# Kernel optimization log

Hardware: AMD Instinct MI355X
Metric: run time of the kernel (lower is better)

Reference implementation:

```python
import jax, jax.numpy as jnp
import numpy as np

ALPHA = 0.95
GAMMA = 8.0
REFRACTORY_STEPS = 2.0
THETA_INC = 0.35
THETA_DECAY = 0.995

B, N, T = 16, 2048, 1000


def setup_inputs() -> dict:
    key = jax.random.key(0)
    u = jax.random.normal(key, (B, N, T), dtype=jnp.float32)
    theta_base = jnp.ones((1, N, 1), dtype=jnp.float32)
    return {"u": u, "theta_base": theta_base}


def surrogate_spike(x):
    # forward: Heaviside (x >= 0); surrogate grad handled in fwdbwd module
    return (x >= 0).astype(x.dtype)


def reference(u, theta_base):
    # u: [B, N, T]; theta_base: [1, N, 1]
    b, n, t = u.shape
    tb = theta_base[0, :, 0]  # [N], broadcasts over batch
    v0 = jnp.zeros((b, n), dtype=u.dtype)
    theta0 = jnp.broadcast_to(tb, (b, n)).astype(u.dtype)
    ref0 = jnp.zeros((b, n), dtype=u.dtype)

    def step(carry, u_t):
        v, theta_dyn, ref = carry
        ref_active = (ref > 0).astype(u_t.dtype)
        u_eff = u_t * (1.0 - ref_active)
        v = ALPHA * v + u_eff
        theta = theta_dyn  # adaptive_theta=True
        s = surrogate_spike(v - theta)
        v = v - s * theta  # soft reset (hard_reset=False)
        ref = jnp.maximum(ref - 1.0, 0.0)
        ref = jnp.where(s > 0, jnp.full_like(ref, REFRACTORY_STEPS), ref)
        theta_dyn = theta_dyn * THETA_DECAY + tb * (1.0 - THETA_DECAY) + THETA_INC * s
        return (v, theta_dyn, ref), (s, v)

    u_t_first = jnp.transpose(u, (2, 0, 1))  # [T, B, N]
    _, (spikes, v_hist) = jax.lax.scan(step, (v0, theta0, ref0), u_t_first)
    spikes = jnp.transpose(spikes, (1, 2, 0))  # [B, N, T]
    v_hist = jnp.transpose(v_hist, (1, 2, 0))
    return spikes, v_hist
```

## Files before the change

kernel.cpp:

```cpp
#include <hip/hip_runtime.h>


constexpr int B_ = 16;
constexpr int N_ = 2048;
constexpr int T_ = 1000;
constexpr int CHUNK = 64;
constexpr int NF4 = CHUNK / 4;
constexpr int NFULL = 15;
constexpr int NPAIR = 7;
constexpr int TAIL_T0 = NFULL * CHUNK;
constexpr int TAIL_F4 = (T_ - TAIL_T0) / 4;

#define LDS_BARRIER()                                          \
    do {                                                       \
        asm volatile("s_waitcnt lgkmcnt(0)" ::: "memory");     \
        __builtin_amdgcn_s_barrier();                          \
    } while (0)

__global__ __launch_bounds__(192) void lif_kernel(
    const float* __restrict__ u,
    const float* __restrict__ theta_base,
    float* __restrict__ spikes,
    float* __restrict__ vhist)
{
    __shared__ float4 s_lds[2][64][NF4];
    __shared__ float4 v_lds[2][64][NF4];

    const int lane = threadIdx.x & 63;
    const int wid = threadIdx.x >> 6;
    const int blk0 = blockIdx.x * 64;
    const size_t row = (size_t)(blk0 + lane) * T_;

    if (wid == 0) {
        const float tb = theta_base[(blk0 + lane) & (N_ - 1)];
        const float c5 = __fmul_rn(tb, 0.005f);
        float v = 0.0f, theta = tb, ref = 0.0f;
        const float* up = u + row;

        float4 bufA[NF4], bufB[NF4];

        auto load_full = [&](float4 (&buf)[NF4], int t0) {
#pragma unroll
            for (int i = 0; i < NF4; ++i)
                buf[i] = *reinterpret_cast<const float4*>(up + t0 + 4 * i);
        };
        auto load_tail = [&](float4 (&buf)[NF4]) {
#pragma unroll
            for (int i = 0; i < TAIL_F4; ++i)
                buf[i] = *reinterpret_cast<const float4*>(up + TAIL_T0 + 4 * i);
        };

        auto step4 = [&](const float4 u4, int par, int tf) {
            const float uin[4] = {u4.x, u4.y, u4.z, u4.w};
            float so[4], vo[4];
#pragma unroll
            for (int k = 0; k < 4; ++k) {
                const float ueff = (ref > 0.0f) ? 0.0f : uin[k];
                v = __fadd_rn(__fmul_rn(0.95f, v), ueff);
                const float d = __fsub_rn(v, theta);
                const bool s = (d >= 0.0f);
                v = s ? __fsub_rn(v, theta) : v;
                ref = fmaxf(__fsub_rn(ref, 1.0f), 0.0f);
                ref = s ? 2.0f : ref;
                theta = __fadd_rn(__fmul_rn(theta, 0.995f), c5);
                theta = s ? __fadd_rn(theta, 0.35f) : theta;

                so[k] = s ? 1.0f : 0.0f;
                vo[k] = v;
            }
            const int ptf = tf ^ (lane & 15);
            s_lds[par][lane][ptf] = make_float4(so[0], so[1], so[2], so[3]);
            v_lds[par][lane][ptf] = make_float4(vo[0], vo[1], vo[2], vo[3]);
        };

        auto process_full = [&](const float4 (&buf)[NF4], int par) {
#pragma unroll
            for (int tf = 0; tf < NF4; ++tf) step4(buf[tf], par, tf);
        };
        auto process_tail = [&](const float4 (&buf)[NF4], int par) {
#pragma unroll
            for (int tf = 0; tf < TAIL_F4; ++tf) step4(buf[tf], par, tf);
        };

        load_full(bufA, 0);
        int t = 0;
#pragma unroll 1
        for (int p = 0; p < NPAIR; ++p) {
            load_full(bufB, t + CHUNK);
            process_full(bufA, 0);
            LDS_BARRIER();
            t += CHUNK;
            load_full(bufA, t + CHUNK);
            process_full(bufB, 1);
            LDS_BARRIER();
            t += CHUNK;
        }
        load_tail(bufB);
        process_full(bufA, 0);
        LDS_BARRIER();
        process_tail(bufB, 1);
        LDS_BARRIER();
    } else {
        float* gout = (wid == 1) ? spikes : vhist;
        const float4 (*src)[64][NF4] = (wid == 1) ? s_lds : v_lds;
        float* gp = gout + (size_t)blk0 * T_;

        const int tf = lane & 15;
        const int rsub = lane >> 4;

#pragma unroll 1
        for (int c = 0; c < NFULL + 1; ++c) {
            if (c > 0) {
                const int par = (c - 1) & 1;
                const int t0 = (c - 1) * CHUNK;
#pragma unroll
                for (int k = 0; k < 16; ++k) {
                    const int r = 4 * k + rsub;
                    const float4 w = src[par][r][tf ^ (r & 15)];
                    *reinterpret_cast<float4*>(gp + (size_t)r * T_ + t0 + 4 * tf) = w;
                }
            }
            LDS_BARRIER();
        }
        {
#pragma unroll
            for (int j = 0; j < TAIL_F4; ++j) {
                const float4 w = src[1][lane][j ^ (lane & 15)];
                *reinterpret_cast<float4*>(gp + (size_t)lane * T_ + TAIL_T0 + 4 * j) = w;
            }
        }
    }
}

extern "C" void kernel_launch(void* const* d_in, const int* in_sizes, int n_in,
                              void* d_out, int out_size, void* d_ws, size_t ws_size,
                              hipStream_t stream) {
    const float* u = (const float*)d_in[0];
    const float* theta_base = (const float*)d_in[1];
    float* out = (float*)d_out;
    float* spikes = out;
    float* vhist = out + (size_t)B_ * N_ * T_;

    const int grid = (B_ * N_) / 64;
    lif_kernel<<<grid, 192, 0, stream>>>(u, theta_base, spikes, vhist);
}
```

Before: 109.8 us.

## Move input loads to a dedicated wave using async global-to-LDS triple buffering

Wave 1 now issues direct global-to-LDS loads of u for a three-deep ring of 32-step chunks, with coalesced row-group access and XOR swizzling. Wave 0 only reads from LDS and runs the recurrence, and wave 2 writes both spikes and v_hist. The aim is to keep the serial compute wave from stalling on strided per-row global loads and to free its registers. In exchange the chunks are half the size, so there are twice as many block barriers, and one writer wave now handles both outputs.

```diff
diff --git a/kernel.cpp b/kernel.cpp
--- a/kernel.cpp
+++ b/kernel.cpp
@@ -4,10 +4,9 @@
 constexpr int B_ = 16;
 constexpr int N_ = 2048;
 constexpr int T_ = 1000;
-constexpr int CHUNK = 64;
+constexpr int CHUNK = 32;
 constexpr int NF4 = CHUNK / 4;
-constexpr int NFULL = 15;
-constexpr int NPAIR = 7;
+constexpr int NFULL = 31;
 constexpr int TAIL_T0 = NFULL * CHUNK;
 constexpr int TAIL_F4 = (T_ - TAIL_T0) / 4;
 
@@ -15,7 +14,14 @@
     do {                                                       \
         asm volatile("s_waitcnt lgkmcnt(0)" ::: "memory");     \
         __builtin_amdgcn_s_barrier();                          \
+        __builtin_amdgcn_sched_barrier(0);                     \
     } while (0)
+
+__device__ __forceinline__ void gload_lds16(const float* g, void* lds) {
+    __builtin_amdgcn_global_load_lds(
+        (const __attribute__((address_space(1))) void*)g,
+        (__attribute__((address_space(3))) void*)lds, 16, 0, 0);
+}
 
 __global__ __launch_bounds__(192) void lif_kernel(
     const float* __restrict__ u,
@@ -23,34 +29,21 @@
     float* __restrict__ spikes,
     float* __restrict__ vhist)
 {
-    __shared__ float4 s_lds[2][64][NF4];
-    __shared__ float4 v_lds[2][64][NF4];
+    __shared__ float4 u_lds[3][64][NF4];
+    __shared__ float4 s_lds[3][64][NF4];
+    __shared__ float4 v_lds[3][64][NF4];
 
     const int lane = threadIdx.x & 63;
     const int wid = threadIdx.x >> 6;
     const int blk0 = blockIdx.x * 64;
-    const size_t row = (size_t)(blk0 + lane) * T_;
 
     if (wid == 0) {
         const float tb = theta_base[(blk0 + lane) & (N_ - 1)];
         const float c5 = __fmul_rn(tb, 0.005f);
         float v = 0.0f, theta = tb, ref = 0.0f;
-        const float* up = u + row;
+        const int sw = lane & 7;
 
-        float4 bufA[NF4], bufB[NF4];
-
-        auto load_full = [&](float4 (&buf)[NF4], int t0) {
-#pragma unroll
-            for (int i = 0; i < NF4; ++i)
-                buf[i] = *reinterpret_cast<const float4*>(up + t0 + 4 * i);
-        };
-        auto load_tail = [&](float4 (&buf)[NF4]) {
-#pragma unroll
-            for (int i = 0; i < TAIL_F4; ++i)
-                buf[i] = *reinterpret_cast<const float4*>(up + TAIL_T0 + 4 * i);
-        };
-
-        auto step4 = [&](const float4 u4, int par, int tf) {
+        auto step4 = [&](const float4 u4, float4& s4, float4& v4) {
             const float uin[4] = {u4.x, u4.y, u4.z, u4.w};
             float so[4], vo[4];
 #pragma unroll
@@ -68,65 +61,123 @@
                 so[k] = s ? 1.0f : 0.0f;
                 vo[k] = v;
             }
-            const int ptf = tf ^ (lane & 15);
-            s_lds[par][lane][ptf] = make_float4(so[0], so[1], so[2], so[3]);
-            v_lds[par][lane][ptf] = make_float4(vo[0], vo[1], vo[2], vo[3]);
+            s4 = make_float4(so[0], so[1], so[2], so[3]);
+            v4 = make_float4(vo[0], vo[1], vo[2], vo[3]);
         };
 
-        auto process_full = [&](const float4 (&buf)[NF4], int par) {
+        __builtin_amdgcn_s_barrier();
+        int bu = 0;
+#pragma unroll 1
+        for (int c = 0; c < NFULL; ++c) {
+            const float4* urow = &u_lds[bu][lane][0];
+            float4* srow = &s_lds[bu][lane][0];
+            float4* vrow = &v_lds[bu][lane][0];
 #pragma unroll
-            for (int tf = 0; tf < NF4; ++tf) step4(buf[tf], par, tf);
+            for (int tf = 0; tf < NF4; ++tf) {
+                float4 s4, v4;
+                step4(urow[tf ^ sw], s4, v4);
+                srow[tf ^ sw] = s4;
+                vrow[tf ^ sw] = v4;
+            }
+            LDS_BARRIER();
+            bu = (bu == 2) ? 0 : bu + 1;
+        }
+        {
+            const float4* ut = &u_lds[bu][0][0];
+            float4* st = &s_lds[bu][0][0];
+            float4* vt = &v_lds[bu][0][0];
+#pragma unroll
+            for (int tf = 0; tf < TAIL_F4; ++tf) {
+                float4 s4, v4;
+                step4(ut[TAIL_F4 * lane + tf], s4, v4);
+                st[TAIL_F4 * lane + tf] = s4;
+                vt[TAIL_F4 * lane + tf] = v4;
+            }
+            LDS_BARRIER();
+        }
+    } else if (wid == 1) {
+        const float* ub = u + (size_t)blk0 * T_;
+        const int r0 = lane >> 3;
+        const int sl = lane & 7;
+
+        auto issue_full = [&](int cc, int buf) {
+#pragma unroll
+            for (int k = 0; k < 8; ++k) {
+                const int r = 8 * k + r0;
+                const float* g =
+                    ub + (size_t)r * T_ + CHUNK * cc + 4 * (sl ^ (r & 7));
+                gload_lds16(g, &u_lds[buf][8 * k][0]);
+            }
         };
-        auto process_tail = [&](const float4 (&buf)[NF4], int par) {
+        auto issue_tail = [&]() {
 #pragma unroll
-            for (int tf = 0; tf < TAIL_F4; ++tf) step4(buf[tf], par, tf);
+            for (int j = 0; j < 2; ++j) {
+                const int r = 32 * j + (lane >> 1);
+                const int tf = lane & 1;
+                const float* g = ub + (size_t)r * T_ + TAIL_T0 + 4 * tf;
+                gload_lds16(g, ((float4*)&u_lds[1][0][0]) + 64 * j);
+            }
         };
 
-        load_full(bufA, 0);
-        int t = 0;
-#pragma unroll 1
-        for (int p = 0; p < NPAIR; ++p) {
-            load_full(bufB, t + CHUNK);
-            process_full(bufA, 0);
-            LDS_BARRIER();
-            t += CHUNK;
-            load_full(bufA, t + CHUNK);
-            process_full(bufB, 1);
-            LDS_BARRIER();
-            t += CHUNK;
-        }
-        load_tail(bufB);
-        process_full(bufA, 0);
-        LDS_BARRIER();
-        process_tail(bufB, 1);
-        LDS_BARRIER();
-    } else {
-        float* gout = (wid == 1) ? spikes : vhist;
-        const float4 (*src)[64][NF4] = (wid == 1) ? s_lds : v_lds;
-        float* gp = gout + (size_t)blk0 * T_;
-
-        const int tf = lane & 15;
-        const int rsub = lane >> 4;
-
+        issue_full(0, 0);
+        issue_full(1, 1);
+        asm volatile("s_waitcnt vmcnt(8)" ::: "memory");
+        __builtin_amdgcn_sched_barrier(0);
+        __builtin_amdgcn_s_barrier();
 #pragma unroll 1
         for (int c = 0; c < NFULL + 1; ++c) {
-            if (c > 0) {
-                const int par = (c - 1) & 1;
-                const int t0 = (c - 1) * CHUNK;
+            if (c <= 28) {
+                issue_full(c + 2, (c + 2) % 3);
+                asm volatile("s_waitcnt vmcnt(8)" ::: "memory");
+            } else if (c == 29) {
+                issue_tail();
+                asm volatile("s_waitcnt vmcnt(2)" ::: "memory");
+            } else if (c == 30) {
+                asm volatile("s_waitcnt vmcnt(0)" ::: "memory");
+            }
+            __builtin_amdgcn_sched_barrier(0);
+            __builtin_amdgcn_s_barrier();
+            __builtin_amdgcn_sched_barrier(0);
+        }
+    } else {
+        float* gs = spikes + (size_t)blk0 * T_;
+        float* gv = vhist + (size_t)blk0 * T_;
+        const int r0 = lane >> 3;
+        const int tfp = lane & 7;
+
+        __builtin_amdgcn_s_barrier();
+#pragma unroll 1
+        for (int c = 0; c < NFULL + 1; ++c) {
+            if (c >= 1) {
+                const int cc = c - 1;
+                const int buf = cc % 3;
+                const int t0 = CHUNK * cc;
 #pragma unroll
-                for (int k = 0; k < 16; ++k) {
-                    const int r = 4 * k + rsub;
-                    const float4 w = src[par][r][tf ^ (r & 15)];
-                    *reinterpret_cast<float4*>(gp + (size_t)r * T_ + t0 + 4 * tf) = w;
+                for (int k = 0; k < 8; ++k) {
+                    const int r = 8 * k + r0;
+                    const float4 w = s_lds[buf][r][tfp ^ (r & 7)];
+                    *(float4*)(gs + (size_t)r * T_ + t0 + 4 * tfp) = w;
+                }
+#pragma unroll
+                for (int k = 0; k < 8; ++k) {
+                    const int r = 8 * k + r0;
+                    const float4 w = v_lds[buf][r][tfp ^ (r & 7)];
+                    *(float4*)(gv + (size_t)r * T_ + t0 + 4 * tfp) = w;
                 }
             }
             LDS_BARRIER();
         }
         {
+            const float4* st = &s_lds[1][0][0];
+            const float4* vt = &v_lds[1][0][0];
 #pragma unroll
-            for (int j = 0; j < TAIL_F4; ++j) {
-                const float4 w = src[1][lane][j ^ (lane & 15)];
-                *reinterpret_cast<float4*>(gp + (size_t)lane * T_ + TAIL_T0 + 4 * j) = w;
+            for (int j = 0; j < 2; ++j) {
+                const int r = 32 * j + (lane >> 1);
+                const int tf = lane & 1;
+                *(float4*)(gs + (size_t)r * T_ + TAIL_T0 + 4 * tf) =
+                    st[64 * j + lane];
+                *(float4*)(gv + (size_t)r * T_ + TAIL_T0 + 4 * tf) =
+                    vt[64 * j + lane];
             }
         }
     }
```

Result: slower. 126.8 us (+15.4%).

## Pack spikes as bitmasks in LDS and drain 128-step chunks from 4-slot ring

Applied to the files above, without the earlier changes.

The compute wave now writes spikes as 64-bit bitmasks per row per 64-step chunk instead of float4s, which cuts LDS traffic for spikes. Voltage goes into a 4-slot LDS ring buffer. The two writer waves now drain two chunks (128 time steps) every other phase, so each row's store segment is 512 bytes rather than 256. This aims to give better global write coalescing and fewer writer iterations, at the cost of more LDS and of expanding the bits back to floats in the spike writer.

```diff
diff --git a/kernel.cpp b/kernel.cpp
--- a/kernel.cpp
+++ b/kernel.cpp
@@ -4,17 +4,16 @@
 constexpr int B_ = 16;
 constexpr int N_ = 2048;
 constexpr int T_ = 1000;
-constexpr int CHUNK = 64;
-constexpr int NF4 = CHUNK / 4;
-constexpr int NFULL = 15;
-constexpr int NPAIR = 7;
-constexpr int TAIL_T0 = NFULL * CHUNK;
-constexpr int TAIL_F4 = (T_ - TAIL_T0) / 4;
+constexpr int Q = 64;
+constexpr int QF4 = Q / 4;
+constexpr int NPH = 16;
+constexpr int TAIL_F4 = 10;
 
 #define LDS_BARRIER()                                          \
     do {                                                       \
         asm volatile("s_waitcnt lgkmcnt(0)" ::: "memory");     \
         __builtin_amdgcn_s_barrier();                          \
+        __builtin_amdgcn_sched_barrier(0);                     \
     } while (0)
 
 __global__ __launch_bounds__(192) void lif_kernel(
@@ -23,36 +22,36 @@
     float* __restrict__ spikes,
     float* __restrict__ vhist)
 {
-    __shared__ float4 s_lds[2][64][NF4];
-    __shared__ float4 v_lds[2][64][NF4];
+    __shared__ float4 v_ring[4][64][QF4];
+    __shared__ uint2  s_bits[4][64];
 
     const int lane = threadIdx.x & 63;
     const int wid = threadIdx.x >> 6;
     const int blk0 = blockIdx.x * 64;
-    const size_t row = (size_t)(blk0 + lane) * T_;
 
     if (wid == 0) {
         const float tb = theta_base[(blk0 + lane) & (N_ - 1)];
         const float c5 = __fmul_rn(tb, 0.005f);
         float v = 0.0f, theta = tb, ref = 0.0f;
-        const float* up = u + row;
-
-        float4 bufA[NF4], bufB[NF4];
-
-        auto load_full = [&](float4 (&buf)[NF4], int t0) {
-#pragma unroll
-            for (int i = 0; i < NF4; ++i)
-                buf[i] = *reinterpret_cast<const float4*>(up + t0 + 4 * i);
-        };
-        auto load_tail = [&](float4 (&buf)[NF4]) {
+        const float* up = u + (size_t)(blk0 + lane) * T_;
+        const int swz = lane & 15;
+
+        float4 bufA[QF4], bufB[QF4];
+
+        auto load_q = [&](float4 (&b)[QF4], int t0) {
+#pragma unroll
+            for (int i = 0; i < QF4; ++i)
+                b[i] = *reinterpret_cast<const float4*>(up + t0 + 4 * i);
+        };
+        auto load_tail = [&](float4 (&b)[QF4]) {
 #pragma unroll
             for (int i = 0; i < TAIL_F4; ++i)
-                buf[i] = *reinterpret_cast<const float4*>(up + TAIL_T0 + 4 * i);
-        };
-
-        auto step4 = [&](const float4 u4, int par, int tf) {
+                b[i] = *reinterpret_cast<const float4*>(up + 15 * Q + 4 * i);
+        };
+
+        auto stepf4 = [&](const float4 u4, unsigned& bw, int sh) -> float4 {
             const float uin[4] = {u4.x, u4.y, u4.z, u4.w};
-            float so[4], vo[4];
+            float vo[4];
 #pragma unroll
             for (int k = 0; k < 4; ++k) {
                 const float ueff = (ref > 0.0f) ? 0.0f : uin[k];
@@ -65,68 +64,140 @@
                 theta = __fadd_rn(__fmul_rn(theta, 0.995f), c5);
                 theta = s ? __fadd_rn(theta, 0.35f) : theta;
 
-                so[k] = s ? 1.0f : 0.0f;
+                bw |= (s ? 1u : 0u) << (sh + k);
                 vo[k] = v;
             }
-            const int ptf = tf ^ (lane & 15);
-            s_lds[par][lane][ptf] = make_float4(so[0], so[1], so[2], so[3]);
-            v_lds[par][lane][ptf] = make_float4(vo[0], vo[1], vo[2], vo[3]);
-        };
-
-        auto process_full = [&](const float4 (&buf)[NF4], int par) {
-#pragma unroll
-            for (int tf = 0; tf < NF4; ++tf) step4(buf[tf], par, tf);
-        };
-        auto process_tail = [&](const float4 (&buf)[NF4], int par) {
-#pragma unroll
-            for (int tf = 0; tf < TAIL_F4; ++tf) step4(buf[tf], par, tf);
-        };
-
-        load_full(bufA, 0);
-        int t = 0;
+            return make_float4(vo[0], vo[1], vo[2], vo[3]);
+        };
+
+        auto process_q = [&](const float4 (&b)[QF4], int bq) {
+            unsigned blo = 0, bhi = 0;
+#pragma unroll
+            for (int tf = 0; tf < QF4; ++tf) {
+                float4 v4 = (tf < 8) ? stepf4(b[tf], blo, 4 * tf)
+                                     : stepf4(b[tf], bhi, 4 * (tf - 8));
+                v_ring[bq][lane][tf ^ swz] = v4;
+            }
+            s_bits[bq][lane] = make_uint2(blo, bhi);
+        };
+        auto process_tail = [&](const float4 (&b)[QF4], int bq) {
+            unsigned blo = 0, bhi = 0;
+#pragma unroll
+            for (int tf = 0; tf < TAIL_F4; ++tf) {
+                float4 v4 = (tf < 8) ? stepf4(b[tf], blo, 4 * tf)
+                                     : stepf4(b[tf], bhi, 4 * (tf - 8));
+                v_ring[bq][lane][tf ^ swz] = v4;
+            }
+            s_bits[bq][lane] = make_uint2(blo, bhi);
+        };
+
+        load_q(bufA, 0);
 #pragma unroll 1
-        for (int p = 0; p < NPAIR; ++p) {
-            load_full(bufB, t + CHUNK);
-            process_full(bufA, 0);
+        for (int p = 0; p < NPH; ++p) {
+            if (!(p & 1)) {
+                if (p < 14) load_q(bufB, (p + 1) * Q);
+                else if (p == 14) load_tail(bufB);
+                process_q(bufA, p & 3);
+            } else {
+                if (p < 15) {
+                    load_q(bufA, (p + 1) * Q);
+                    process_q(bufB, p & 3);
+                } else {
+                    process_tail(bufB, 3);
+                }
+            }
             LDS_BARRIER();
-            t += CHUNK;
-            load_full(bufA, t + CHUNK);
-            process_full(bufB, 1);
+        }
+    } else if (wid == 1) {
+        float* gv = vhist + (size_t)blk0 * T_;
+        const int jj = lane & 31;
+        const int half = lane >> 5;
+
+#pragma unroll 1
+        for (int p = 0; p < NPH; ++p) {
+            if (p >= 2 && !(p & 1)) {
+                const int t0 = (p - 2) * Q;
+                const int b0 = (p - 2) & 3;
+                const int bq = (b0 + (jj >> 4)) & 3;
+                const int slb = jj & 15;
+#pragma unroll
+                for (int k = 0; k < 32; ++k) {
+                    const int R = 2 * k + half;
+                    const float4 w = v_ring[bq][R][slb ^ (R & 15)];
+                    *(float4*)(gv + (size_t)R * T_ + t0 + 4 * jj) = w;
+                }
+            }
             LDS_BARRIER();
-            t += CHUNK;
-        }
-        load_tail(bufB);
-        process_full(bufA, 0);
-        LDS_BARRIER();
-        process_tail(bufB, 1);
-        LDS_BARRIER();
+        }
+        {
+            const int r0 = lane >> 4, tf = lane & 15;
+#pragma unroll
+            for (int k = 0; k < 16; ++k) {
+                const int R = 4 * k + r0;
+                const float4 w = v_ring[2][R][tf ^ (R & 15)];
+                *(float4*)(gv + (size_t)R * T_ + 14 * Q + 4 * tf) = w;
+            }
+        }
+        {
+#pragma unroll
+            for (int tf = 0; tf < TAIL_F4; ++tf) {
+                const float4 w = v_ring[3][lane][tf ^ (lane & 15)];
+                *(float4*)(gv + (size_t)lane * T_ + 15 * Q + 4 * tf) = w;
+            }
+        }
     } else {
-        float* gout = (wid == 1) ? spikes : vhist;
-        const float4 (*src)[64][NF4] = (wid == 1) ? s_lds : v_lds;
-        float* gp = gout + (size_t)blk0 * T_;
-
-        const int tf = lane & 15;
-        const int rsub = lane >> 4;
+        float* gs = spikes + (size_t)blk0 * T_;
+        const int jj = lane & 31;
+        const int half = lane >> 5;
+
+        auto expand = [](unsigned w, int ob) -> float4 {
+            float4 f;
+            f.x = ((w >> (ob + 0)) & 1u) ? 1.0f : 0.0f;
+            f.y = ((w >> (ob + 1)) & 1u) ? 1.0f : 0.0f;
+            f.z = ((w >> (ob + 2)) & 1u) ? 1.0f : 0.0f;
+            f.w = ((w >> (ob + 3)) & 1u) ? 1.0f : 0.0f;
+            return f;
+        };
 
 #pragma unroll 1
-        for (int c = 0; c < NFULL + 1; ++c) {
-            if (c > 0) {
-                const int par = (c - 1) & 1;
-                const int t0 = (c - 1) * CHUNK;
-#pragma unroll
-                for (int k = 0; k < 16; ++k) {
-                    const int r = 4 * k + rsub;
-                    const float4 w = src[par][r][tf ^ (r & 15)];
-                    *reinterpret_cast<float4*>(gp + (size_t)r * T_ + t0 + 4 * tf) = w;
+        for (int p = 0; p < NPH; ++p) {
+            if (p >= 2 && !(p & 1)) {
+                const int t0 = (p - 2) * Q;
+                const int b0 = (p - 2) & 3;
+                const int bq = (b0 + (jj >> 4)) & 3;
+                const int wq = (jj & 15) >> 3;
+                const int ob = 4 * (jj & 7);
+#pragma unroll
+                for (int k = 0; k < 32; ++k) {
+                    const int R = 2 * k + half;
+                    const uint2 bw = s_bits[bq][R];
+                    const unsigned w = wq ? bw.y : bw.x;
+                    *(float4*)(gs + (size_t)R * T_ + t0 + 4 * jj) =
+                        expand(w, ob);
                 }
             }
             LDS_BARRIER();
         }
         {
-#pragma unroll
-            for (int j = 0; j < TAIL_F4; ++j) {
-                const float4 w = src[1][lane][j ^ (lane & 15)];
-                *reinterpret_cast<float4*>(gp + (size_t)lane * T_ + TAIL_T0 + 4 * j) = w;
+            const int r0 = lane >> 4, tf = lane & 15;
+            const int wq = tf >> 3;
+            const int ob = 4 * (tf & 7);
+#pragma unroll
+            for (int k = 0; k < 16; ++k) {
+                const int R = 4 * k + r0;
+                const uint2 bw = s_bits[2][R];
+                const unsigned w = wq ? bw.y : bw.x;
+                *(float4*)(gs + (size_t)R * T_ + 14 * Q + 4 * tf) =
+                    expand(w, ob);
+            }
+        }
+        {
+            const uint2 bw = s_bits[3][lane];
+#pragma unroll
+            for (int tf = 0; tf < TAIL_F4; ++tf) {
+                const unsigned w = (tf >> 3) ? bw.y : bw.x;
+                *(float4*)(gs + (size_t)lane * T_ + 15 * Q + 4 * tf) =
+                    expand(w, 4 * (tf & 7));
             }
         }
     }
```

After: 126.9 us. +15.5%, slower.
